# Performance work log

Measured on AMD Instinct MI355X. Metric: run time of the kernel, lower is better.

The kernel has to match this reference:

```python
import jax, jax.numpy as jnp
import numpy as np

EMB = 1024
HEADS = 16
HEAD_DIM = EMB // HEADS


def setup_inputs() -> dict:
    key = jax.random.key(0)
    ks = jax.random.split(key, 6)
    B, T, D = 4, 2048, EMB
    s = 1.0 / np.sqrt(D)
    return {
        "x": jax.random.normal(ks[0], (B, T, D), dtype=jnp.float32),
        "Wq": jax.random.normal(ks[1], (D, D), dtype=jnp.float32) * s,
        "Wk": jax.random.normal(ks[2], (D, D), dtype=jnp.float32) * s,
        "Wv": jax.random.normal(ks[3], (D, D), dtype=jnp.float32) * s,
        "Wo": jax.random.normal(ks[4], (D, D), dtype=jnp.float32) * s,
        "bo": jax.random.normal(ks[5], (D,), dtype=jnp.float32) * 0.01,
    }


def reference(x, Wq, Wk, Wv, Wo, bo):
    B, T, D = x.shape
    H, Hd = HEADS, HEAD_DIM
    # torch Linear: x @ W.T ; here W stored [out,in]
    def heads(W):
        return (x @ W.T).reshape(B, T, H, Hd).transpose(0, 2, 1, 3)  # [B,H,T,Hd]
    Q, K, V = heads(Wq), heads(Wk), heads(Wv)
    scores = jnp.einsum("bhqd,bhkd->bhqk", Q, K) / np.sqrt(Hd)
    causal = jnp.triu(jnp.ones((T, T), dtype=bool), k=1)
    scores = jnp.where(causal, -jnp.inf, scores)
    weights = jax.nn.softmax(scores, axis=-1)  # dropout rate 0 -> identity
    ctx = jnp.einsum("bhqk,bhkd->bhqd", weights, V)
    ctx = ctx.transpose(0, 2, 1, 3).reshape(B, T, D)
    return ctx @ Wo.T + bo
```

## Files before the change

### kernel.cpp

```cpp
#include <hip/hip_runtime.h>

typedef short bf16x8 __attribute__((ext_vector_type(8)));
typedef float f32x4 __attribute__((ext_vector_type(4)));
typedef unsigned short u16;
typedef unsigned int u32;

__device__ __forceinline__ u16 f2b(float x) {
  union { float f; u32 u; } c; c.f = x;
  u32 r = (c.u + 0x7FFFu + ((c.u >> 16) & 1u)) >> 16;
  return (u16)r;
}

__device__ __forceinline__ float fexp2(float x) {
  return __builtin_amdgcn_exp2f(x);
}

__device__ __forceinline__ void glds16(const void* g, void* l) {
  __builtin_amdgcn_global_load_lds(
      (const __attribute__((address_space(1))) u32*)g,
      (__attribute__((address_space(3))) u32*)l, 16, 0, 0);
}

__global__ void cvt_all(const float* __restrict__ x, const float* __restrict__ Wq,
                        const float* __restrict__ Wk, const float* __restrict__ Wv,
                        const float* __restrict__ Wo, u16* __restrict__ xb,
                        u16* __restrict__ wqkvb, u16* __restrict__ wob, float qscale) {
  const int i = blockIdx.x * blockDim.x + threadIdx.x;
  const float* src;
  u16* dst;
  float scale = 1.0f;
  int off;
  if (i < 2097152) {
    src = x; dst = xb; off = i;
  } else {
    const int j = i - 2097152;
    const int wsel = j >> 18;
    off = j & 262143;
    if (wsel == 0)      { src = Wq; dst = wqkvb;            scale = qscale; }
    else if (wsel == 1) { src = Wk; dst = wqkvb + 1048576; }
    else if (wsel == 2) { src = Wv; dst = wqkvb + 2097152; }
    else                { src = Wo; dst = wob; }
  }
  float4 v = reinterpret_cast<const float4*>(src)[off];
  ushort4 o;
  o.x = f2b(v.x * scale); o.y = f2b(v.y * scale);
  o.z = f2b(v.z * scale); o.w = f2b(v.w * scale);
  reinterpret_cast<ushort4*>(dst)[off] = o;
}

template<int MODE>
__global__ __launch_bounds__(512, 2)
void gemm2(const u16* __restrict__ A, const u16* __restrict__ Bm,
           u16* __restrict__ Cq, u16* __restrict__ Ck, u16* __restrict__ Cvt,
           float* __restrict__ Cf, const float* __restrict__ bias) {
  constexpr int K = 1024, NKT = K / 64;
  __shared__ __attribute__((aligned(16))) u16 lds[3][24576];
  const int tid = threadIdx.x;
  const int w = tid >> 6;
  const int l = tid & 63;
  const int wm = w >> 2, wn = w & 3;
  const int lr = l & 15, lg = l >> 4;
  const int brow = blockIdx.x * 128;
  const int bcol = blockIdx.y * 256;
  const int wg = w * 64;

  const u16* Ab = A + (size_t)brow * K;
  const u16* Bb = Bm + (size_t)bcol * K;
  int gA[2], lA[2], gB[4], lB[4];
#pragma unroll
  for (int i = 0; i < 2; ++i) {
    const int q = i * 512 + tid;
    const int r = q >> 3, s = (q & 7) ^ (r & 7);
    gA[i] = r * K + s * 8;
    lA[i] = (i * 512 + wg) * 8;
  }
#pragma unroll
  for (int i = 0; i < 4; ++i) {
    const int q = i * 512 + tid;
    const int r = q >> 3, s = (q & 7) ^ (r & 7);
    gB[i] = r * K + s * 8;
    lB[i] = 8192 + (i * 512 + wg) * 8;
  }

  int aoff[4][2], boff[4][2];
#pragma unroll
  for (int m = 0; m < 4; ++m) {
    const int row = wm * 64 + m * 16 + lr;
#pragma unroll
    for (int kk = 0; kk < 2; ++kk)
      aoff[m][kk] = row * 64 + (((kk * 4 + lg) ^ (row & 7)) * 8);
  }
#pragma unroll
  for (int n = 0; n < 4; ++n) {
    const int row = wn * 64 + n * 16 + lr;
#pragma unroll
    for (int kk = 0; kk < 2; ++kk)
      boff[n][kk] = 8192 + row * 64 + (((kk * 4 + lg) ^ (row & 7)) * 8);
  }

  f32x4 acc[4][4] = {};

#pragma unroll
  for (int i = 0; i < 2; ++i) glds16(Ab + gA[i], &lds[0][lA[i]]);
#pragma unroll
  for (int i = 0; i < 4; ++i) glds16(Bb + gB[i], &lds[0][lB[i]]);
#pragma unroll
  for (int i = 0; i < 2; ++i) glds16(Ab + gA[i] + 64, &lds[1][lA[i]]);
#pragma unroll
  for (int i = 0; i < 4; ++i) glds16(Bb + gB[i] + 64, &lds[1][lB[i]]);
  asm volatile("s_waitcnt vmcnt(6)" ::: "memory");
  asm volatile("s_barrier" ::: "memory");

  int bi = 0;
  for (int kt = 0; kt < NKT; ++kt) {
    const u16* Lb = lds[bi];
    const int bs = (bi + 2 >= 3) ? (bi - 1) : (bi + 2);
    const bool st = (kt + 2 < NKT);
    const int ko = (kt + 2) * 64;

    bf16x8 a[4][2], b01[2][2];
#pragma unroll
    for (int m = 0; m < 4; ++m)
#pragma unroll
      for (int kk = 0; kk < 2; ++kk)
        a[m][kk] = *reinterpret_cast<const bf16x8*>(&Lb[aoff[m][kk]]);
#pragma unroll
    for (int n = 0; n < 2; ++n)
#pragma unroll
      for (int kk = 0; kk < 2; ++kk)
        b01[n][kk] = *reinterpret_cast<const bf16x8*>(&Lb[boff[n][kk]]);
    if (st) {
      glds16(Ab + gA[0] + ko, &lds[bs][lA[0]]);
      glds16(Ab + gA[1] + ko, &lds[bs][lA[1]]);
      glds16(Bb + gB[0] + ko, &lds[bs][lB[0]]);
    }
    asm volatile("s_barrier" ::: "memory");
    asm volatile("s_waitcnt lgkmcnt(0)" ::: "memory");
    __builtin_amdgcn_sched_barrier(0);
    __builtin_amdgcn_s_setprio(1);
#pragma unroll
    for (int m = 0; m < 4; ++m)
#pragma unroll
      for (int n = 0; n < 2; ++n)
#pragma unroll
        for (int kk = 0; kk < 2; ++kk)
          acc[m][n] = __builtin_amdgcn_mfma_f32_16x16x32_bf16(a[m][kk], b01[n][kk], acc[m][n], 0, 0, 0);
    __builtin_amdgcn_s_setprio(0);
    asm volatile("s_barrier" ::: "memory");

    bf16x8 b23[2][2];
#pragma unroll
    for (int n = 0; n < 2; ++n)
#pragma unroll
      for (int kk = 0; kk < 2; ++kk)
        b23[n][kk] = *reinterpret_cast<const bf16x8*>(&Lb[boff[n + 2][kk]]);
    if (st) {
      glds16(Bb + gB[1] + ko, &lds[bs][lB[1]]);
      glds16(Bb + gB[2] + ko, &lds[bs][lB[2]]);
      glds16(Bb + gB[3] + ko, &lds[bs][lB[3]]);
    }
    if (kt + 1 < NKT) {
      if (st) asm volatile("s_waitcnt vmcnt(6)" ::: "memory");
      else    asm volatile("s_waitcnt vmcnt(0)" ::: "memory");
    }
    asm volatile("s_barrier" ::: "memory");
    asm volatile("s_waitcnt lgkmcnt(0)" ::: "memory");
    __builtin_amdgcn_sched_barrier(0);
    __builtin_amdgcn_s_setprio(1);
#pragma unroll
    for (int m = 0; m < 4; ++m)
#pragma unroll
      for (int n = 0; n < 2; ++n)
#pragma unroll
        for (int kk = 0; kk < 2; ++kk)
          acc[m][n + 2] = __builtin_amdgcn_mfma_f32_16x16x32_bf16(a[m][kk], b23[n][kk], acc[m][n + 2], 0, 0, 0);
    __builtin_amdgcn_s_setprio(0);
    asm volatile("s_barrier" ::: "memory");

    bi = (bi + 1 >= 3) ? 0 : bi + 1;
  }

  if (MODE == 0) {
    const int seg = blockIdx.y >> 2;
    const int cbase = (blockIdx.y & 3) * 256;
    if (seg < 2) {
      u16* dst = (seg == 0) ? Cq : Ck;
#pragma unroll
      for (int m = 0; m < 4; ++m) {
        const size_t r = (size_t)(brow + wm * 64 + m * 16 + lg * 4);
#pragma unroll
        for (int n = 0; n < 4; ++n) {
          const int c = cbase + wn * 64 + n * 16 + lr;
#pragma unroll
          for (int j = 0; j < 4; ++j)
            dst[(r + j) * 1024 + c] = f2b(acc[m][n][j]);
        }
      }
    } else {
#pragma unroll
      for (int n = 0; n < 4; ++n) {
        const int c = cbase + wn * 64 + n * 16 + lr;
        const int hh = c >> 6, dd = c & 63;
#pragma unroll
        for (int m = 0; m < 4; ++m) {
          const int r0 = brow + wm * 64 + m * 16 + lg * 4;
#pragma unroll
          for (int j = 0; j < 4; ++j) {
            const int r = r0 + j;
            const int bt = r >> 11, tt = r & 2047;
            Cvt[((size_t)((bt * 16 + hh) * 64 + dd)) * 2048 + tt] = f2b(acc[m][n][j]);
          }
        }
      }
    }
  } else {
#pragma unroll
    for (int m = 0; m < 4; ++m) {
      const size_t r = (size_t)(brow + wm * 64 + m * 16 + lg * 4);
#pragma unroll
      for (int n = 0; n < 4; ++n) {
        const int c = bcol + wn * 64 + n * 16 + lr;
        const float bv = bias[c];
#pragma unroll
        for (int j = 0; j < 4; ++j)
          Cf[(r + j) * 1024 + c] = acc[m][n][j] + bv;
      }
    }
  }
}

__global__ __launch_bounds__(256, 3)
void attn_kernel(const u16* __restrict__ qb, const u16* __restrict__ kb,
                 const u16* __restrict__ vt, u16* __restrict__ ctx) {
  __shared__ __attribute__((aligned(16))) u16 Ks[2][4096];
  __shared__ __attribute__((aligned(16))) u16 Vs[2][4096];
  __shared__ __attribute__((aligned(16))) u16 Ps[4 * 2048];
  const int bid = blockIdx.x;
  const int qt = 15 - (bid >> 6);
  const int bh = bid & 63;
  const int bb = bh >> 4, h = bh & 15;
  const int tid = threadIdx.x, w = tid >> 6, l = tid & 63;
  const int lr = l & 15, lg = l >> 4;
  const int Qw = qt * 128 + w * 32;
  const int kvr = tid >> 3;
  const int gv = tid & 7;
  const int kvc = gv * 8;
  const int pgW = ((gv ^ (kvr & 7)) * 8);

  int prd[2];
#pragma unroll
  for (int kc = 0; kc < 2; ++kc) prd[kc] = ((kc * 4 + lg) ^ (lr & 7)) * 8;

  bf16x8 qf[2][2];
#pragma unroll
  for (int mi = 0; mi < 2; ++mi)
#pragma unroll
    for (int kc = 0; kc < 2; ++kc)
      qf[mi][kc] = *reinterpret_cast<const bf16x8*>(
          &qb[(size_t)(bb * 2048 + Qw + mi * 16 + lr) * 1024 + h * 64 + kc * 32 + lg * 8]);

  f32x4 oacc[2][4] = {};
  float lsum[2][4] = {};

  const int ntiles = 2 * qt + 2;

  bf16x8 kr[2], vr[2];
#pragma unroll
  for (int it = 0; it < 2; ++it) {
    kr[it] = *reinterpret_cast<const bf16x8*>(
        &kb[(size_t)(bb * 2048 + it * 32 + kvr) * 1024 + h * 64 + kvc]);
    vr[it] = *reinterpret_cast<const bf16x8*>(
        &vt[(size_t)(bh * 64 + it * 32 + kvr) * 2048 + kvc]);
  }
#pragma unroll
  for (int it = 0; it < 2; ++it) {
    *reinterpret_cast<bf16x8*>(&Ks[0][(it * 32 + kvr) * 64 + pgW]) = kr[it];
    *reinterpret_cast<bf16x8*>(&Vs[0][(it * 32 + kvr) * 64 + pgW]) = vr[it];
  }
  __syncthreads();
#pragma unroll
  for (int it = 0; it < 2; ++it) {
    kr[it] = *reinterpret_cast<const bf16x8*>(
        &kb[(size_t)(bb * 2048 + 64 + it * 32 + kvr) * 1024 + h * 64 + kvc]);
    vr[it] = *reinterpret_cast<const bf16x8*>(
        &vt[(size_t)(bh * 64 + it * 32 + kvr) * 2048 + 64 + kvc]);
  }

  for (int t = 0; t < ntiles; ++t) {
    const int c0 = t * 64;
    const int cur = t & 1;

    if (c0 < Qw + 32) {
      const bool diag = (c0 + 63 > Qw);

      f32x4 sacc[2][4] = {};
      __builtin_amdgcn_s_setprio(1);
#pragma unroll
      for (int kc = 0; kc < 2; ++kc)
#pragma unroll
        for (int nj = 0; nj < 4; ++nj) {
          bf16x8 kf = *reinterpret_cast<const bf16x8*>(
              &Ks[cur][(nj * 16 + lr) * 64 + prd[kc]]);
#pragma unroll
          for (int mi = 0; mi < 2; ++mi)
            sacc[mi][nj] = __builtin_amdgcn_mfma_f32_16x16x32_bf16(qf[mi][kc], kf, sacc[mi][nj], 0, 0, 0);
        }
      __builtin_amdgcn_s_setprio(0);

#pragma unroll
      for (int mi = 0; mi < 2; ++mi) {
        if (diag) {
#pragma unroll
          for (int nj = 0; nj < 4; ++nj) {
            const int col = c0 + nj * 16 + lr;
#pragma unroll
            for (int j = 0; j < 4; ++j) {
              const int row = Qw + mi * 16 + lg * 4 + j;
              if (col > row) sacc[mi][nj][j] = -1e30f;
            }
          }
        }
#pragma unroll
        for (int nj = 0; nj < 4; ++nj) {
          const int cchunk = nj * 2 + (lr >> 3);
          const int coff = lr & 7;
#pragma unroll
          for (int j = 0; j < 4; ++j) {
            const float p = fexp2(sacc[mi][nj][j]);
            lsum[mi][j] += p;
            const int rowP = mi * 16 + lg * 4 + j;
            Ps[w * 2048 + rowP * 64 + ((cchunk ^ (rowP & 7)) * 8) + coff] = f2b(p);
          }
        }
      }

      __builtin_amdgcn_s_setprio(1);
#pragma unroll
      for (int kc = 0; kc < 2; ++kc) {
        bf16x8 pf[2];
#pragma unroll
        for (int mi = 0; mi < 2; ++mi) {
          const int rowP = mi * 16 + lr;
          const int cj = kc * 4 + lg;
          pf[mi] = *reinterpret_cast<const bf16x8*>(
              &Ps[w * 2048 + rowP * 64 + ((cj ^ (rowP & 7)) * 8)]);
        }
#pragma unroll
        for (int nd = 0; nd < 4; ++nd) {
          bf16x8 vf = *reinterpret_cast<const bf16x8*>(
              &Vs[cur][(nd * 16 + lr) * 64 + prd[kc]]);
#pragma unroll
          for (int mi = 0; mi < 2; ++mi)
            oacc[mi][nd] = __builtin_amdgcn_mfma_f32_16x16x32_bf16(pf[mi], vf, oacc[mi][nd], 0, 0, 0);
        }
      }
      __builtin_amdgcn_s_setprio(0);
    }

    if (t + 1 < ntiles) {
#pragma unroll
      for (int it = 0; it < 2; ++it) {
        *reinterpret_cast<bf16x8*>(&Ks[cur ^ 1][(it * 32 + kvr) * 64 + pgW]) = kr[it];
        *reinterpret_cast<bf16x8*>(&Vs[cur ^ 1][(it * 32 + kvr) * 64 + pgW]) = vr[it];
      }
    }
    __syncthreads();
    if (t + 2 < ntiles) {
      const int c0n = c0 + 128;
#pragma unroll
      for (int it = 0; it < 2; ++it) {
        kr[it] = *reinterpret_cast<const bf16x8*>(
            &kb[(size_t)(bb * 2048 + c0n + it * 32 + kvr) * 1024 + h * 64 + kvc]);
        vr[it] = *reinterpret_cast<const bf16x8*>(
            &vt[(size_t)(bh * 64 + it * 32 + kvr) * 2048 + c0n + kvc]);
      }
    }
  }

#pragma unroll
  for (int mi = 0; mi < 2; ++mi) {
#pragma unroll
    for (int x = 1; x < 16; x <<= 1)
#pragma unroll
      for (int j = 0; j < 4; ++j) lsum[mi][j] += __shfl_xor(lsum[mi][j], x, 64);
#pragma unroll
    for (int j = 0; j < 4; ++j) {
      const float inv = 1.0f / lsum[mi][j];
      const size_t r = (size_t)(bb * 2048 + Qw + mi * 16 + lg * 4 + j);
#pragma unroll
      for (int nd = 0; nd < 4; ++nd)
        ctx[r * 1024 + h * 64 + nd * 16 + lr] = f2b(oacc[mi][nd][j] * inv);
    }
  }
}

extern "C" void kernel_launch(void* const* d_in, const int* in_sizes, int n_in,
                              void* d_out, int out_size, void* d_ws, size_t ws_size,
                              hipStream_t stream) {
  const float* x = (const float*)d_in[0];
  const float* Wq = (const float*)d_in[1];
  const float* Wk = (const float*)d_in[2];
  const float* Wv = (const float*)d_in[3];
  const float* Wo = (const float*)d_in[4];
  const float* bo = (const float*)d_in[5];
  float* out = (float*)d_out;

  char* ws = (char*)d_ws;
  u16* xb = (u16*)(ws);
  u16* qb = (u16*)(ws + (16u << 20));
  u16* kb = (u16*)(ws + (32u << 20));
  u16* vtb = (u16*)(ws + (64u << 20));
  u16* wqkvb = (u16*)(ws + (80u << 20));
  u16* wob = (u16*)(ws + (88u << 20));

  const float qscale = 0.125f * 1.4426950408889634f;
  cvt_all<<<12288, 256, 0, stream>>>(x, Wq, Wk, Wv, Wo, xb, wqkvb, wob, qscale);

  gemm2<0><<<dim3(64, 12), 512, 0, stream>>>(xb, wqkvb, qb, kb, vtb, nullptr, nullptr);
  attn_kernel<<<1024, 256, 0, stream>>>(qb, kb, vtb, xb);
  gemm2<1><<<dim3(64, 4), 512, 0, stream>>>(xb, wob, nullptr, nullptr, nullptr, out, bo);
}
```

Baseline: 157.0 us.

## Fuse fp32-to-bf16 conversion of x into the QKV GEMM A-tile loads

The QKV GEMM now loads x directly in fp32 through registers, converts it to bf16, and writes it swizzled into LDS inside the pipelined K loop. This removes the separate pass that converted x to bf16 and wrote it back to memory, and the conversion kernel now handles only the weights. In exchange, the GEMM reads twice the A bytes (fp32), and each of the 12 column blocks converts the same A tile again. It also uses more registers for the prefetch buffers and needs a more intricate vmcnt schedule.

```diff
diff --git a/kernel.cpp b/kernel.cpp
--- a/kernel.cpp
+++ b/kernel.cpp
@@ -21,26 +21,32 @@
       (__attribute__((address_space(3))) u32*)l, 16, 0, 0);
 }
 
-__global__ void cvt_all(const float* __restrict__ x, const float* __restrict__ Wq,
-                        const float* __restrict__ Wk, const float* __restrict__ Wv,
-                        const float* __restrict__ Wo, u16* __restrict__ xb,
-                        u16* __restrict__ wqkvb, u16* __restrict__ wob, float qscale) {
+__device__ __forceinline__ f32x4 gload4(const float* p) {
+  f32x4 r;
+  asm volatile("global_load_dwordx4 %0, %1, off" : "=v"(r) : "v"(p) : "memory");
+  return r;
+}
+
+__device__ __forceinline__ void cvt_write(u16* dst, const f32x4 a, const f32x4 b) {
+  bf16x8 v;
+#pragma unroll
+  for (int j = 0; j < 4; ++j) { v[j] = (short)f2b(a[j]); v[4 + j] = (short)f2b(b[j]); }
+  *reinterpret_cast<bf16x8*>(dst) = v;
+}
+
+__global__ void cvt_w(const float* __restrict__ Wq, const float* __restrict__ Wk,
+                      const float* __restrict__ Wv, const float* __restrict__ Wo,
+                      u16* __restrict__ wqkvb, u16* __restrict__ wob, float qscale) {
   const int i = blockIdx.x * blockDim.x + threadIdx.x;
+  const int wsel = i >> 18;
+  const int off = i & 262143;
   const float* src;
   u16* dst;
   float scale = 1.0f;
-  int off;
-  if (i < 2097152) {
-    src = x; dst = xb; off = i;
-  } else {
-    const int j = i - 2097152;
-    const int wsel = j >> 18;
-    off = j & 262143;
-    if (wsel == 0)      { src = Wq; dst = wqkvb;            scale = qscale; }
-    else if (wsel == 1) { src = Wk; dst = wqkvb + 1048576; }
-    else if (wsel == 2) { src = Wv; dst = wqkvb + 2097152; }
-    else                { src = Wo; dst = wob; }
-  }
+  if (wsel == 0)      { src = Wq; dst = wqkvb;            scale = qscale; }
+  else if (wsel == 1) { src = Wk; dst = wqkvb + 1048576; }
+  else if (wsel == 2) { src = Wv; dst = wqkvb + 2097152; }
+  else                { src = Wo; dst = wob; }
   float4 v = reinterpret_cast<const float4*>(src)[off];
   ushort4 o;
   o.x = f2b(v.x * scale); o.y = f2b(v.y * scale);
@@ -50,7 +56,8 @@
 
 template<int MODE>
 __global__ __launch_bounds__(512, 2)
-void gemm2(const u16* __restrict__ A, const u16* __restrict__ Bm,
+void gemm2(const float* __restrict__ Af32, const u16* __restrict__ Ab16,
+           const u16* __restrict__ Bm,
            u16* __restrict__ Cq, u16* __restrict__ Ck, u16* __restrict__ Cvt,
            float* __restrict__ Cf, const float* __restrict__ bias) {
   constexpr int K = 1024, NKT = K / 64;
@@ -64,16 +71,8 @@
   const int bcol = blockIdx.y * 256;
   const int wg = w * 64;
 
-  const u16* Ab = A + (size_t)brow * K;
   const u16* Bb = Bm + (size_t)bcol * K;
-  int gA[2], lA[2], gB[4], lB[4];
-#pragma unroll
-  for (int i = 0; i < 2; ++i) {
-    const int q = i * 512 + tid;
-    const int r = q >> 3, s = (q & 7) ^ (r & 7);
-    gA[i] = r * K + s * 8;
-    lA[i] = (i * 512 + wg) * 8;
-  }
+  int gB[4], lB[4];
 #pragma unroll
   for (int i = 0; i < 4; ++i) {
     const int q = i * 512 + tid;
@@ -99,85 +98,191 @@
   }
 
   f32x4 acc[4][4] = {};
-
-#pragma unroll
-  for (int i = 0; i < 2; ++i) glds16(Ab + gA[i], &lds[0][lA[i]]);
-#pragma unroll
-  for (int i = 0; i < 4; ++i) glds16(Bb + gB[i], &lds[0][lB[i]]);
-#pragma unroll
-  for (int i = 0; i < 2; ++i) glds16(Ab + gA[i] + 64, &lds[1][lA[i]]);
-#pragma unroll
-  for (int i = 0; i < 4; ++i) glds16(Bb + gB[i] + 64, &lds[1][lB[i]]);
-  asm volatile("s_waitcnt vmcnt(6)" ::: "memory");
-  asm volatile("s_barrier" ::: "memory");
-
   int bi = 0;
-  for (int kt = 0; kt < NKT; ++kt) {
-    const u16* Lb = lds[bi];
-    const int bs = (bi + 2 >= 3) ? (bi - 1) : (bi + 2);
-    const bool st = (kt + 2 < NKT);
-    const int ko = (kt + 2) * 64;
-
-    bf16x8 a[4][2], b01[2][2];
-#pragma unroll
-    for (int m = 0; m < 4; ++m)
-#pragma unroll
-      for (int kk = 0; kk < 2; ++kk)
-        a[m][kk] = *reinterpret_cast<const bf16x8*>(&Lb[aoff[m][kk]]);
-#pragma unroll
-    for (int n = 0; n < 2; ++n)
-#pragma unroll
-      for (int kk = 0; kk < 2; ++kk)
-        b01[n][kk] = *reinterpret_cast<const bf16x8*>(&Lb[boff[n][kk]]);
-    if (st) {
-      glds16(Ab + gA[0] + ko, &lds[bs][lA[0]]);
-      glds16(Ab + gA[1] + ko, &lds[bs][lA[1]]);
-      glds16(Bb + gB[0] + ko, &lds[bs][lB[0]]);
-    }
+
+  if constexpr (MODE == 0) {
+    const float* Af = Af32 + (size_t)brow * K;
+    const int r0 = tid >> 3, c0 = tid & 7;
+    const int r1 = 64 + r0;
+    const size_t aof0 = (size_t)r0 * K + c0 * 8;
+    const size_t aof1 = (size_t)r1 * K + c0 * 8;
+    const int aw0 = r0 * 64 + ((c0 ^ (r0 & 7)) * 8);
+    const int aw1 = r1 * 64 + ((c0 ^ (r1 & 7)) * 8);
+
+    f32x4 rE[4], rO[4], t0[4], t1[4];
+    t0[0] = gload4(Af + aof0);      t0[1] = gload4(Af + aof0 + 4);
+    t0[2] = gload4(Af + aof1);      t0[3] = gload4(Af + aof1 + 4);
+    t1[0] = gload4(Af + aof0 + 64); t1[1] = gload4(Af + aof0 + 68);
+    t1[2] = gload4(Af + aof1 + 64); t1[3] = gload4(Af + aof1 + 68);
+    rE[0] = gload4(Af + aof0 + 128); rE[1] = gload4(Af + aof0 + 132);
+    rE[2] = gload4(Af + aof1 + 128); rE[3] = gload4(Af + aof1 + 132);
+#pragma unroll
+    for (int i = 0; i < 4; ++i) glds16(Bb + gB[i], &lds[0][lB[i]]);
+#pragma unroll
+    for (int i = 0; i < 4; ++i) glds16(Bb + gB[i] + 64, &lds[1][lB[i]]);
+    asm volatile("s_waitcnt vmcnt(12)" ::: "memory");
+    __builtin_amdgcn_sched_barrier(0);
+    cvt_write(&lds[0][aw0], t0[0], t0[1]);
+    cvt_write(&lds[0][aw1], t0[2], t0[3]);
+    cvt_write(&lds[1][aw0], t1[0], t1[1]);
+    cvt_write(&lds[1][aw1], t1[2], t1[3]);
+    asm volatile("s_waitcnt vmcnt(4)" ::: "memory");
+    asm volatile("s_waitcnt lgkmcnt(0)" ::: "memory");
     asm volatile("s_barrier" ::: "memory");
-    asm volatile("s_waitcnt lgkmcnt(0)" ::: "memory");
-    __builtin_amdgcn_sched_barrier(0);
-    __builtin_amdgcn_s_setprio(1);
-#pragma unroll
-    for (int m = 0; m < 4; ++m)
+
+#define GSTEP(KT, RC, RL)                                                      \
+  {                                                                            \
+    const u16* Lb = lds[bi];                                                   \
+    const int bs = (bi + 2 >= 3) ? (bi - 1) : (bi + 2);                        \
+    const int ko = ((KT) + 2) * 64;                                            \
+    bf16x8 a[4][2], b01[2][2];                                                 \
+    _Pragma("unroll") for (int m = 0; m < 4; ++m)                              \
+      _Pragma("unroll") for (int kk = 0; kk < 2; ++kk)                         \
+        a[m][kk] = *reinterpret_cast<const bf16x8*>(&Lb[aoff[m][kk]]);         \
+    _Pragma("unroll") for (int n = 0; n < 2; ++n)                              \
+      _Pragma("unroll") for (int kk = 0; kk < 2; ++kk)                         \
+        b01[n][kk] = *reinterpret_cast<const bf16x8*>(&Lb[boff[n][kk]]);       \
+    if ((KT) + 2 < NKT) glds16(Bb + gB[0] + ko, &lds[bs][lB[0]]);              \
+    if ((KT) + 3 < NKT) {                                                      \
+      const float* Ap = Af + ((KT) + 3) * 64;                                  \
+      RL[0] = gload4(Ap + aof0); RL[1] = gload4(Ap + aof0 + 4);                \
+      RL[2] = gload4(Ap + aof1); RL[3] = gload4(Ap + aof1 + 4);                \
+    }                                                                          \
+    asm volatile("s_barrier" ::: "memory");                                    \
+    asm volatile("s_waitcnt lgkmcnt(0)" ::: "memory");                         \
+    __builtin_amdgcn_sched_barrier(0);                                         \
+    __builtin_amdgcn_s_setprio(1);                                             \
+    _Pragma("unroll") for (int m = 0; m < 4; ++m)                              \
+      _Pragma("unroll") for (int n = 0; n < 2; ++n)                            \
+        _Pragma("unroll") for (int kk = 0; kk < 2; ++kk)                       \
+          acc[m][n] = __builtin_amdgcn_mfma_f32_16x16x32_bf16(                 \
+              a[m][kk], b01[n][kk], acc[m][n], 0, 0, 0);                       \
+    __builtin_amdgcn_s_setprio(0);                                             \
+    asm volatile("s_barrier" ::: "memory");                                    \
+    bf16x8 b23[2][2];                                                          \
+    _Pragma("unroll") for (int n = 0; n < 2; ++n)                              \
+      _Pragma("unroll") for (int kk = 0; kk < 2; ++kk)                         \
+        b23[n][kk] = *reinterpret_cast<const bf16x8*>(&Lb[boff[n + 2][kk]]);   \
+    if ((KT) + 2 < NKT) {                                                      \
+      glds16(Bb + gB[1] + ko, &lds[bs][lB[1]]);                                \
+      glds16(Bb + gB[2] + ko, &lds[bs][lB[2]]);                                \
+      glds16(Bb + gB[3] + ko, &lds[bs][lB[3]]);                                \
+    }                                                                          \
+    if ((KT) + 3 < NKT)      asm volatile("s_waitcnt vmcnt(8)" ::: "memory");  \
+    else if ((KT) + 2 < NKT) asm volatile("s_waitcnt vmcnt(4)" ::: "memory");  \
+    else if ((KT) + 1 < NKT) asm volatile("s_waitcnt vmcnt(0)" ::: "memory");  \
+    __builtin_amdgcn_sched_barrier(0);                                         \
+    if ((KT) + 2 < NKT) {                                                      \
+      cvt_write(&lds[bs][aw0], RC[0], RC[1]);                                  \
+      cvt_write(&lds[bs][aw1], RC[2], RC[3]);                                  \
+    }                                                                          \
+    asm volatile("s_barrier" ::: "memory");                                    \
+    asm volatile("s_waitcnt lgkmcnt(0)" ::: "memory");                         \
+    __builtin_amdgcn_sched_barrier(0);                                         \
+    __builtin_amdgcn_s_setprio(1);                                             \
+    _Pragma("unroll") for (int m = 0; m < 4; ++m)                              \
+      _Pragma("unroll") for (int n = 0; n < 2; ++n)                            \
+        _Pragma("unroll") for (int kk = 0; kk < 2; ++kk)                       \
+          acc[m][n + 2] = __builtin_amdgcn_mfma_f32_16x16x32_bf16(             \
+              a[m][kk], b23[n][kk], acc[m][n + 2], 0, 0, 0);                   \
+    __builtin_amdgcn_s_setprio(0);                                             \
+    asm volatile("s_barrier" ::: "memory");                                    \
+    bi = (bi + 1 >= 3) ? 0 : bi + 1;                                           \
+  }
+
+    for (int kt = 0; kt < NKT; kt += 2) {
+      GSTEP(kt, rE, rO);
+      GSTEP(kt + 1, rO, rE);
+    }
+#undef GSTEP
+  } else {
+    const u16* Ab = Ab16 + (size_t)brow * K;
+    int gA[2], lA[2];
+#pragma unroll
+    for (int i = 0; i < 2; ++i) {
+      const int q = i * 512 + tid;
+      const int r = q >> 3, s = (q & 7) ^ (r & 7);
+      gA[i] = r * K + s * 8;
+      lA[i] = (i * 512 + wg) * 8;
+    }
+#pragma unroll
+    for (int i = 0; i < 2; ++i) glds16(Ab + gA[i], &lds[0][lA[i]]);
+#pragma unroll
+    for (int i = 0; i < 4; ++i) glds16(Bb + gB[i], &lds[0][lB[i]]);
+#pragma unroll
+    for (int i = 0; i < 2; ++i) glds16(Ab + gA[i] + 64, &lds[1][lA[i]]);
+#pragma unroll
+    for (int i = 0; i < 4; ++i) glds16(Bb + gB[i] + 64, &lds[1][lB[i]]);
+    asm volatile("s_waitcnt vmcnt(6)" ::: "memory");
+    asm volatile("s_barrier" ::: "memory");
+
+    for (int kt = 0; kt < NKT; ++kt) {
+      const u16* Lb = lds[bi];
+      const int bs = (bi + 2 >= 3) ? (bi - 1) : (bi + 2);
+      const bool st = (kt + 2 < NKT);
+      const int ko = (kt + 2) * 64;
+
+      bf16x8 a[4][2], b01[2][2];
+#pragma unroll
+      for (int m = 0; m < 4; ++m)
+#pragma unroll
+        for (int kk = 0; kk < 2; ++kk)
+          a[m][kk] = *reinterpret_cast<const bf16x8*>(&Lb[aoff[m][kk]]);
 #pragma unroll
       for (int n = 0; n < 2; ++n)
 #pragma unroll
         for (int kk = 0; kk < 2; ++kk)
-          acc[m][n] = __builtin_amdgcn_mfma_f32_16x16x32_bf16(a[m][kk], b01[n][kk], acc[m][n], 0, 0, 0);
-    __builtin_amdgcn_s_setprio(0);
-    asm volatile("s_barrier" ::: "memory");
-
-    bf16x8 b23[2][2];
-#pragma unroll
-    for (int n = 0; n < 2; ++n)
-#pragma unroll
-      for (int kk = 0; kk < 2; ++kk)
-        b23[n][kk] = *reinterpret_cast<const bf16x8*>(&Lb[boff[n + 2][kk]]);
-    if (st) {
-      glds16(Bb + gB[1] + ko, &lds[bs][lB[1]]);
-      glds16(Bb + gB[2] + ko, &lds[bs][lB[2]]);
-      glds16(Bb + gB[3] + ko, &lds[bs][lB[3]]);
-    }
-    if (kt + 1 < NKT) {
-      if (st) asm volatile("s_waitcnt vmcnt(6)" ::: "memory");
-      else    asm volatile("s_waitcnt vmcnt(0)" ::: "memory");
-    }
-    asm volatile("s_barrier" ::: "memory");
-    asm volatile("s_waitcnt lgkmcnt(0)" ::: "memory");
-    __builtin_amdgcn_sched_barrier(0);
-    __builtin_amdgcn_s_setprio(1);
-#pragma unroll
-    for (int m = 0; m < 4; ++m)
+          b01[n][kk] = *reinterpret_cast<const bf16x8*>(&Lb[boff[n][kk]]);
+      if (st) {
+        glds16(Ab + gA[0] + ko, &lds[bs][lA[0]]);
+        glds16(Ab + gA[1] + ko, &lds[bs][lA[1]]);
+        glds16(Bb + gB[0] + ko, &lds[bs][lB[0]]);
+      }
+      asm volatile("s_barrier" ::: "memory");
+      asm volatile("s_waitcnt lgkmcnt(0)" ::: "memory");
+      __builtin_amdgcn_sched_barrier(0);
+      __builtin_amdgcn_s_setprio(1);
+#pragma unroll
+      for (int m = 0; m < 4; ++m)
+#pragma unroll
+        for (int n = 0; n < 2; ++n)
+#pragma unroll
+          for (int kk = 0; kk < 2; ++kk)
+            acc[m][n] = __builtin_amdgcn_mfma_f32_16x16x32_bf16(a[m][kk], b01[n][kk], acc[m][n], 0, 0, 0);
+      __builtin_amdgcn_s_setprio(0);
+      asm volatile("s_barrier" ::: "memory");
+
+      bf16x8 b23[2][2];
 #pragma unroll
       for (int n = 0; n < 2; ++n)
 #pragma unroll
         for (int kk = 0; kk < 2; ++kk)
-          acc[m][n + 2] = __builtin_amdgcn_mfma_f32_16x16x32_bf16(a[m][kk], b23[n][kk], acc[m][n + 2], 0, 0, 0);
-    __builtin_amdgcn_s_setprio(0);
-    asm volatile("s_barrier" ::: "memory");
-
-    bi = (bi + 1 >= 3) ? 0 : bi + 1;
+          b23[n][kk] = *reinterpret_cast<const bf16x8*>(&Lb[boff[n + 2][kk]]);
+      if (st) {
+        glds16(Bb + gB[1] + ko, &lds[bs][lB[1]]);
+        glds16(Bb + gB[2] + ko, &lds[bs][lB[2]]);
+        glds16(Bb + gB[3] + ko, &lds[bs][lB[3]]);
+      }
+      if (kt + 1 < NKT) {
+        if (st) asm volatile("s_waitcnt vmcnt(6)" ::: "memory");
+        else    asm volatile("s_waitcnt vmcnt(0)" ::: "memory");
+      }
+      asm volatile("s_barrier" ::: "memory");
+      asm volatile("s_waitcnt lgkmcnt(0)" ::: "memory");
+      __builtin_amdgcn_sched_barrier(0);
+      __builtin_amdgcn_s_setprio(1);
+#pragma unroll
+      for (int m = 0; m < 4; ++m)
+#pragma unroll
+        for (int n = 0; n < 2; ++n)
+#pragma unroll
+          for (int kk = 0; kk < 2; ++kk)
+            acc[m][n + 2] = __builtin_amdgcn_mfma_f32_16x16x32_bf16(a[m][kk], b23[n][kk], acc[m][n + 2], 0, 0, 0);
+      __builtin_amdgcn_s_setprio(0);
+      asm volatile("s_barrier" ::: "memory");
+
+      bi = (bi + 1 >= 3) ? 0 : bi + 1;
+    }
   }
 
   if (MODE == 0) {
@@ -406,7 +511,7 @@
   float* out = (float*)d_out;
 
   char* ws = (char*)d_ws;
-  u16* xb = (u16*)(ws);
+  u16* ctxb = (u16*)(ws);
   u16* qb = (u16*)(ws + (16u << 20));
   u16* kb = (u16*)(ws + (32u << 20));
   u16* vtb = (u16*)(ws + (64u << 20));
@@ -414,9 +519,9 @@
   u16* wob = (u16*)(ws + (88u << 20));
 
   const float qscale = 0.125f * 1.4426950408889634f;
-  cvt_all<<<12288, 256, 0, stream>>>(x, Wq, Wk, Wv, Wo, xb, wqkvb, wob, qscale);
-
-  gemm2<0><<<dim3(64, 12), 512, 0, stream>>>(xb, wqkvb, qb, kb, vtb, nullptr, nullptr);
-  attn_kernel<<<1024, 256, 0, stream>>>(qb, kb, vtb, xb);
-  gemm2<1><<<dim3(64, 4), 512, 0, stream>>>(xb, wob, nullptr, nullptr, nullptr, out, bo);
-}
+  cvt_w<<<4096, 256, 0, stream>>>(Wq, Wk, Wv, Wo, wqkvb, wob, qscale);
+
+  gemm2<0><<<dim3(64, 12), 512, 0, stream>>>(x, nullptr, wqkvb, qb, kb, vtb, nullptr, nullptr);
+  attn_kernel<<<1024, 256, 0, stream>>>(qb, kb, vtb, ctxb);
+  gemm2<1><<<dim3(64, 4), 512, 0, stream>>>(nullptr, ctxb, wob, nullptr, nullptr, nullptr, out, bo);
+}
```

Measured after the change: 164.2 us. +4.6%, slower.
